# Performance work log

Hardware: AMD Instinct MI355X
Metric: run time of the kernel (lower is better)

## Reference

```python
import jax, jax.numpy as jnp
import numpy as np

Z, Y, X = 32, 480, 480          # sparse voxel grid (LiDAR-scale)
N = 200_000                     # active voxels
C_IN, C_OUT = 64, 64
EPS = 1e-5


def _subm_conv(f, nbr, w):
    """Submanifold sparse conv as gather-matmul-accumulate.
    f: [N, Cin]; nbr: [N, K] neighbor row ids, pad index == N for missing;
    w: [K, Cin, Cout]."""
    f_pad = jnp.concatenate([f, jnp.zeros((1, f.shape[1]), f.dtype)], axis=0)
    g = f_pad[nbr]                       # [N, K, Cin] gathered neighbor features
    return jnp.einsum('nkc,kco->no', g, w)


def _bn(x, gamma, beta):
    # BatchNorm1d in training mode: batch stats over the N dimension
    m = x.mean(axis=0)
    v = x.var(axis=0)
    return (x - m) * jax.lax.rsqrt(v + EPS) * gamma + beta


def setup_inputs() -> dict:
    rng = np.random.default_rng(0)
    ids = rng.choice(Z * Y * X, size=N, replace=False)
    lookup = np.full(Z * Y * X, -1, dtype=np.int64)
    lookup[ids] = np.arange(N)
    z = ids // (Y * X)
    y = (ids // X) % Y
    x = ids % X

    def nbr_table(offsets):
        cols = []
        for dz, dy, dx in offsets:
            zz, yy, xx = z + dz, y + dy, x + dx
            ok = (zz >= 0) & (zz < Z) & (yy >= 0) & (yy < Y) & (xx >= 0) & (xx < X)
            lin = np.clip((zz * Y + yy) * X + xx, 0, Z * Y * X - 1)
            idx = np.where(ok, lookup[lin], -1)
            cols.append(np.where(idx >= 0, idx, N))   # pad index N -> zero row
        return jnp.asarray(np.stack(cols, axis=1).astype(np.int32))

    off13 = [(0, dy, dx) for dy in (-1, 0, 1) for dx in (-1, 0, 1)]  # kernel (1,3,3)
    off31 = [(dz, 0, dx) for dz in (-1, 0, 1) for dx in (-1, 0, 1)]  # kernel (3,1,3)

    key = jax.random.key(0)
    ks = jax.random.split(key, 5)
    s = 0.05
    ones = jnp.ones((C_OUT,), jnp.float32)
    zeros = jnp.zeros((C_OUT,), jnp.float32)
    return {
        'features': jax.random.normal(ks[0], (N, C_IN), jnp.float32),
        'w1':   jax.random.normal(ks[1], (9, C_IN, C_OUT), jnp.float32) * s,
        'w1_2': jax.random.normal(ks[2], (9, C_OUT, C_OUT), jnp.float32) * s,
        'w2':   jax.random.normal(ks[3], (9, C_IN, C_OUT), jnp.float32) * s,
        'w3':   jax.random.normal(ks[4], (9, C_OUT, C_OUT), jnp.float32) * s,
        'g0': ones, 'b0': zeros, 'g0_2': ones, 'b0_2': zeros,
        'g1': ones, 'b1': zeros, 'g2': ones, 'b2': zeros,
        'nbr13': nbr_table(off13),
        'nbr31': nbr_table(off31),
    }


def reference(features, w1, w1_2, w2, w3, g0, b0, g0_2, b0_2, g1, b1, g2, b2,
              nbr13, nbr31):
    # shortcut branch: conv1x3 -> LeakyReLU -> BN -> conv3x1 -> LeakyReLU -> BN
    sc = _subm_conv(features, nbr13, w1)
    sc = _bn(jax.nn.leaky_relu(sc), g0, b0)
    sc = _subm_conv(sc, nbr31, w1_2)
    sc = _bn(jax.nn.leaky_relu(sc), g0_2, b0_2)
    # main branch: conv3x1 -> LeakyReLU -> BN -> conv1x3 -> LeakyReLU -> BN
    r = _subm_conv(features, nbr31, w2)
    r = _bn(jax.nn.leaky_relu(r), g1, b1)
    r = _subm_conv(r, nbr13, w3)
    r = _bn(jax.nn.leaky_relu(r), g2, b2)
    return r + sc
```

## Files before the change

### kernel.cpp

```cpp
#include <hip/hip_runtime.h>

#define NVOX 200000
#define TM 128
#define NBLK 1563
#define NREP 32
#define STG 4224

typedef unsigned short u16;
typedef unsigned int u32;
typedef __bf16 bf16x8 __attribute__((ext_vector_type(8)));
typedef float f32x16 __attribute__((ext_vector_type(16)));

__device__ __forceinline__ float bf2f(u16 h) { return __uint_as_float(((u32)h) << 16); }
__device__ __forceinline__ u16 f2bf(float x) {
  u32 u = __float_as_uint(x);
  u32 r = u + 0x7fffu + ((u >> 16) & 1u);
  return (u16)(r >> 16);
}
__device__ __forceinline__ uint4 cvt8(uint4 a, uint4 b) {
  const float* fa = (const float*)&a;
  const float* fb = (const float*)&b;
  uint4 r;
  u16* q = (u16*)&r;
#pragma unroll
  for (int j = 0; j < 4; ++j) { q[j] = f2bf(fa[j]); q[4 + j] = f2bf(fb[j]); }
  return r;
}

template <int PHASE>
__global__ __launch_bounds__(256, 6)
void conv_fused(const void* __restrict__ inA, const void* __restrict__ inB,
                const int* __restrict__ nbrA, const int* __restrict__ nbrB,
                const u16* __restrict__ wfA, const u16* __restrict__ wfB,
                void* yA, void* yB, float* __restrict__ stA, float* __restrict__ stB) {
  __shared__ __align__(16) float fb4[64 * 68];
  __shared__ float sred[4][128];

  const int tid = threadIdx.x;
  const int bid = blockIdx.x;
  const bool hB = (bid >= NBLK);
  const int blk = hB ? bid - NBLK : bid;
  const void* f = hB ? inB : inA;
  const int* nbr = hB ? nbrB : nbrA;
  const u16* wf = hB ? wfB : wfA;
  float* st = hB ? stB : stA;

  const int wv = tid >> 6;
  const int lane = tid & 63;
  const int lrow = lane & 31;
  const int lq = lane >> 5;
  const int base = blk * TM;
  const int gr = base + wv * 32 + lrow;

  int ids[9];
#pragma unroll
  for (int j = 0; j < 9; ++j) ids[j] = (gr < NVOX) ? nbr[gr * 9 + j] : NVOX;

  f32x16 acc0 = {0.f, 0.f, 0.f, 0.f, 0.f, 0.f, 0.f, 0.f,
                 0.f, 0.f, 0.f, 0.f, 0.f, 0.f, 0.f, 0.f};
  f32x16 acc1 = acc0;
  constexpr bool FOLDED = (PHASE == 1);
  constexpr bool INF32 = (PHASE == 0);
  constexpr int KSTRIDE = FOLDED ? 5120 : 4096;

#pragma unroll
  for (int k = 0; k < 9; ++k) {
    if (k != 4) {
      if (__ballot(ids[k] < NVOX) == 0ull) continue;
    }
    const int id = ids[k];
    const bool ok = id < NVOX;
    uint4 af[4];
    if constexpr (INF32) {
      const float* p = (const float*)f + (size_t)id * 64 + lq * 8;
#pragma unroll
      for (int ksi = 0; ksi < 4; ++ksi) {
        uint4 v0 = make_uint4(0u, 0u, 0u, 0u), v1 = v0;
        if (ok) { v0 = *(const uint4*)(p + ksi * 16); v1 = *(const uint4*)(p + ksi * 16 + 4); }
        af[ksi] = cvt8(v0, v1);
      }
    } else {
      const u16* p = (const u16*)f + (size_t)id * 64 + lq * 8;
#pragma unroll
      for (int ksi = 0; ksi < 4; ++ksi) {
        uint4 v = make_uint4(0u, 0u, 0u, 0u);
        if (ok) v = *(const uint4*)(p + ksi * 16);
        af[ksi] = v;
      }
    }
    const u16* wb = wf + k * KSTRIDE;
#pragma unroll
    for (int ksi = 0; ksi < 4; ++ksi) {
      bf16x8 a = __builtin_bit_cast(bf16x8, af[ksi]);
      bf16x8 b0 = __builtin_bit_cast(bf16x8, *(const uint4*)(wb + (ksi * 2) * 512 + lane * 8));
      bf16x8 b1 = __builtin_bit_cast(bf16x8, *(const uint4*)(wb + (ksi * 2 + 1) * 512 + lane * 8));
      acc0 = __builtin_amdgcn_mfma_f32_32x32x16_bf16(a, b0, acc0, 0, 0, 0);
      acc1 = __builtin_amdgcn_mfma_f32_32x32x16_bf16(a, b1, acc1, 0, 0, 0);
    }
    if constexpr (FOLDED) {
      uint4 a4 = make_uint4(0u, 0u, 0u, 0u);
      if (lq == 0 && ok) ((u16*)&a4)[0] = 0x3F80u;
      bf16x8 a = __builtin_bit_cast(bf16x8, a4);
      bf16x8 b0 = __builtin_bit_cast(bf16x8, *(const uint4*)(wb + 8 * 512 + lane * 8));
      bf16x8 b1 = __builtin_bit_cast(bf16x8, *(const uint4*)(wb + 9 * 512 + lane * 8));
      acc0 = __builtin_amdgcn_mfma_f32_32x32x16_bf16(a, b0, acc0, 0, 0, 0);
      acc1 = __builtin_amdgcn_mfma_f32_32x32x16_bf16(a, b1, acc1, 0, 0, 0);
    }
  }

  const int cc0 = lrow, cc1 = 32 + lrow;
  float s0 = 0.f, q0 = 0.f, s1 = 0.f, q1 = 0.f;
  float vout[2][16];
#pragma unroll
  for (int r = 0; r < 16; ++r) {
    float v = acc0[r]; v = v > 0.f ? v : 0.01f * v;
    s0 += v; q0 += v * v; vout[0][r] = v;
    float w = acc1[r]; w = w > 0.f ? w : 0.01f * w;
    s1 += w; q1 += w * w; vout[1][r] = w;
  }
  s0 += __shfl_xor(s0, 32); q0 += __shfl_xor(q0, 32);
  s1 += __shfl_xor(s1, 32); q1 += __shfl_xor(q1, 32);
  if (lq == 0) {
    sred[wv][lrow] = s0; sred[wv][32 + lrow] = s1;
    sred[wv][64 + lrow] = q0; sred[wv][96 + lrow] = q1;
  }

  const bool f32out = (PHASE == 1) && !hB;
  const int trow = tid >> 3, cp = tid & 7;
  u16* bb = (u16*)fb4;
#pragma unroll
  for (int h = 0; h < 2; ++h) {
    __syncthreads();
    if ((wv >> 1) == h) {
      const int lr = 32 * (wv & 1);
#pragma unroll
      for (int r = 0; r < 16; ++r) {
        int rowD = lr + (r & 3) + 8 * (r >> 2) + 4 * lq;
        if (f32out) {
          fb4[rowD * 68 + cc0] = vout[0][r];
          fb4[rowD * 68 + cc1] = vout[1][r];
        } else {
          bb[rowD * 72 + cc0] = f2bf(vout[0][r]);
          bb[rowD * 72 + cc1] = f2bf(vout[1][r]);
        }
      }
    }
    __syncthreads();
    if (f32out) {
      float* y = (float*)yA;
#pragma unroll
      for (int it = 0; it < 2; ++it) {
        int r = it * 32 + trow, row = base + 64 * h + r;
        if (row < NVOX) {
          *(float4*)(y + (size_t)row * 64 + cp * 8) = *(const float4*)(fb4 + r * 68 + cp * 8);
          *(float4*)(y + (size_t)row * 64 + cp * 8 + 4) = *(const float4*)(fb4 + r * 68 + cp * 8 + 4);
        }
      }
    } else {
      u16* y = (u16*)(hB ? yB : yA);
#pragma unroll
      for (int it = 0; it < 2; ++it) {
        int r = it * 32 + trow, row = base + 64 * h + r;
        if (row < NVOX)
          *(uint4*)(y + (size_t)row * 64 + cp * 8) = *(const uint4*)(bb + r * 72 + cp * 8);
      }
    }
  }
  if (tid < 128) {
    int which = tid >> 6, c = tid & 63;
    float v = sred[0][which * 64 + c] + sred[1][which * 64 + c] +
              sred[2][which * 64 + c] + sred[3][which * 64 + c];
    atomicAdd(&st[(bid & (NREP - 1)) * 128 + which * 64 + c], v);
  }
}

template <bool IN_F32, bool FOLDED, int MODE>
__global__ __launch_bounds__(256, 4)
void conv_k(const void* __restrict__ fv, const int* __restrict__ nbr,
            const u16* __restrict__ wf, void* yv, float* __restrict__ st,
            float* io, const float* __restrict__ affD,
            const float* __restrict__ affB) {
  __shared__ __align__(16) float fb[128 * 68];
  __shared__ float sred[4][128];

  const int tid = threadIdx.x;
  const int wv = tid >> 6;
  const int lane = tid & 63;
  const int lrow = lane & 31;
  const int lq = lane >> 5;
  const int base = blockIdx.x * TM;
  const int gr = base + wv * 32 + lrow;

  int ids[9];
#pragma unroll
  for (int j = 0; j < 9; ++j) ids[j] = (gr < NVOX) ? nbr[gr * 9 + j] : NVOX;

  f32x16 acc0 = {0.f, 0.f, 0.f, 0.f, 0.f, 0.f, 0.f, 0.f,
                 0.f, 0.f, 0.f, 0.f, 0.f, 0.f, 0.f, 0.f};
  f32x16 acc1 = acc0;
  constexpr int KSTRIDE = FOLDED ? 5120 : 4096;

#pragma unroll
  for (int k = 0; k < 9; ++k) {
    if (k != 4) {
      if (__ballot(ids[k] < NVOX) == 0ull) continue;
    }
    const int id = ids[k];
    const bool ok = id < NVOX;
    uint4 af[4];
    if constexpr (IN_F32) {
      const float* p = (const float*)fv + (size_t)id * 64 + lq * 8;
#pragma unroll
      for (int ksi = 0; ksi < 4; ++ksi) {
        uint4 v0 = make_uint4(0u, 0u, 0u, 0u), v1 = v0;
        if (ok) { v0 = *(const uint4*)(p + ksi * 16); v1 = *(const uint4*)(p + ksi * 16 + 4); }
        af[ksi] = cvt8(v0, v1);
      }
    } else {
      const u16* p = (const u16*)fv + (size_t)id * 64 + lq * 8;
#pragma unroll
      for (int ksi = 0; ksi < 4; ++ksi) {
        uint4 v = make_uint4(0u, 0u, 0u, 0u);
        if (ok) v = *(const uint4*)(p + ksi * 16);
        af[ksi] = v;
      }
    }
    const u16* wb = wf + k * KSTRIDE;
#pragma unroll
    for (int ksi = 0; ksi < 4; ++ksi) {
      bf16x8 a = __builtin_bit_cast(bf16x8, af[ksi]);
      bf16x8 b0 = __builtin_bit_cast(bf16x8, *(const uint4*)(wb + (ksi * 2) * 512 + lane * 8));
      bf16x8 b1 = __builtin_bit_cast(bf16x8, *(const uint4*)(wb + (ksi * 2 + 1) * 512 + lane * 8));
      acc0 = __builtin_amdgcn_mfma_f32_32x32x16_bf16(a, b0, acc0, 0, 0, 0);
      acc1 = __builtin_amdgcn_mfma_f32_32x32x16_bf16(a, b1, acc1, 0, 0, 0);
    }
    if constexpr (FOLDED) {
      uint4 a4 = make_uint4(0u, 0u, 0u, 0u);
      if (lq == 0 && ok) ((u16*)&a4)[0] = 0x3F80u;
      bf16x8 a = __builtin_bit_cast(bf16x8, a4);
      bf16x8 b0 = __builtin_bit_cast(bf16x8, *(const uint4*)(wb + 8 * 512 + lane * 8));
      bf16x8 b1 = __builtin_bit_cast(bf16x8, *(const uint4*)(wb + 9 * 512 + lane * 8));
      acc0 = __builtin_amdgcn_mfma_f32_32x32x16_bf16(a, b0, acc0, 0, 0, 0);
      acc1 = __builtin_amdgcn_mfma_f32_32x32x16_bf16(a, b1, acc1, 0, 0, 0);
    }
  }

  const int cc0 = lrow, cc1 = 32 + lrow;
  float aD0 = 0.f, aD1 = 0.f, hD0 = 0.f, hD1 = 0.f;
  if constexpr (MODE == 2) {
    aD0 = affD[cc0]; hD0 = affD[64 + cc0];
    aD1 = affD[cc1]; hD1 = affD[64 + cc1];
  }
  float s0 = 0.f, q0 = 0.f, s1 = 0.f, q1 = 0.f;
  float vout[2][16];
#pragma unroll
  for (int r = 0; r < 16; ++r) {
    float v = acc0[r]; v = v > 0.f ? v : 0.01f * v;
    s0 += v; q0 += v * v; vout[0][r] = v;
    float w = acc1[r]; w = w > 0.f ? w : 0.01f * w;
    s1 += w; q1 += w * w; vout[1][r] = w;
  }
  if constexpr (MODE != 2) {
    s0 += __shfl_xor(s0, 32); q0 += __shfl_xor(q0, 32);
    s1 += __shfl_xor(s1, 32); q1 += __shfl_xor(q1, 32);
    if (lq == 0) {
      sred[wv][lrow] = s0; sred[wv][32 + lrow] = s1;
      sred[wv][64 + lrow] = q0; sred[wv][96 + lrow] = q1;
    }
  }
  if constexpr (MODE == 0) {
    u16* bb = (u16*)fb;
#pragma unroll
    for (int r = 0; r < 16; ++r) {
      int rowD = 32 * wv + (r & 3) + 8 * (r >> 2) + 4 * lq;
      bb[rowD * 72 + cc0] = f2bf(vout[0][r]);
      bb[rowD * 72 + cc1] = f2bf(vout[1][r]);
    }
  } else if constexpr (MODE == 2 || MODE == 3) {
#pragma unroll
    for (int r = 0; r < 16; ++r) {
      int rowD = 32 * wv + (r & 3) + 8 * (r >> 2) + 4 * lq;
      float v0 = vout[0][r], v1 = vout[1][r];
      if constexpr (MODE == 2) { v0 = fmaf(v0, aD0, hD0); v1 = fmaf(v1, aD1, hD1); }
      fb[rowD * 68 + cc0] = v0;
      fb[rowD * 68 + cc1] = v1;
    }
  }
  __syncthreads();

  const int trow = tid >> 3, cp = tid & 7;
  if constexpr (MODE == 0) {
    u16* y = (u16*)yv;
    const u16* bb = (const u16*)fb;
#pragma unroll
    for (int it = 0; it < 4; ++it) {
      int r = it * 32 + trow, row = base + r;
      if (row < NVOX)
        *(uint4*)(y + (size_t)row * 64 + cp * 8) = *(const uint4*)(bb + r * 72 + cp * 8);
    }
  }
  if constexpr (MODE == 3) {
    float* y = (float*)yv;
#pragma unroll
    for (int it = 0; it < 4; ++it) {
      int r = it * 32 + trow, row = base + r;
      if (row < NVOX) {
        *(float4*)(y + (size_t)row * 64 + cp * 8) = *(const float4*)(fb + r * 68 + cp * 8);
        *(float4*)(y + (size_t)row * 64 + cp * 8 + 4) = *(const float4*)(fb + r * 68 + cp * 8 + 4);
      }
    }
  }
  if constexpr (MODE == 2) {
    float* y = (float*)yv;
#pragma unroll
    for (int it = 0; it < 4; ++it) {
      int r = it * 32 + trow, row = base + r;
      if (row < NVOX) {
        float t[8], p[8], o[8];
        *(float4*)&t[0] = *(const float4*)(fb + r * 68 + cp * 8);
        *(float4*)&t[4] = *(const float4*)(fb + r * 68 + cp * 8 + 4);
        *(float4*)&p[0] = *(const float4*)(io + (size_t)row * 64 + cp * 8);
        *(float4*)&p[4] = *(const float4*)(io + (size_t)row * 64 + cp * 8 + 4);
#pragma unroll
        for (int j = 0; j < 8; ++j) {
          int c = cp * 8 + j;
          o[j] = t[j] + fmaf(p[j], affB[c], affB[64 + c]);
        }
        *(float4*)(y + (size_t)row * 64 + cp * 8) = *(const float4*)&o[0];
        *(float4*)(y + (size_t)row * 64 + cp * 8 + 4) = *(const float4*)&o[4];
      }
    }
  }
  if constexpr (MODE != 2) {
    if (tid < 128) {
      int which = tid >> 6, c = tid & 63;
      float v = sred[0][which * 64 + c] + sred[1][which * 64 + c] +
                sred[2][which * 64 + c] + sred[3][which * 64 + c];
      atomicAdd(&st[(blockIdx.x & (NREP - 1)) * 128 + which * 64 + c], v);
    }
  }
}

__global__ void prep_all(const float* __restrict__ feat, const float* __restrict__ w1,
                         const float* __restrict__ w2, u16* __restrict__ wf,
                         u16* __restrict__ F, float* __restrict__ st,
                         int cvt_blocks) {
  const int bid = blockIdx.x, tid = threadIdx.x;
  if (bid < cvt_blocks) {
    int i8 = (bid * 256 + tid) * 8;
    if (i8 < NVOX * 64) {
      uint4 a = *(const uint4*)(feat + i8);
      uint4 b = *(const uint4*)(feat + i8 + 4);
      *(uint4*)(F + i8) = cvt8(a, b);
    }
    return;
  }
  int rb = bid - cvt_blocks;
  if (rb < 288) {
    int e = rb * 256 + tid;
    int slot = e / 36864, r = e % 36864;
    int k = r >> 12, rr = r & 4095;
    int frag = rr >> 9, lane = (rr >> 3) & 63, j = rr & 7;
    int ks = frag >> 1, ct = frag & 1;
    int cin = ks * 16 + (lane >> 5) * 8 + j;
    int cout = ct * 32 + (lane & 31);
    const float* src = slot ? w2 : w1;
    wf[e] = f2bf(src[k * 4096 + cin * 64 + cout]);
    return;
  }
  for (int i = tid; i < 4 * STG; i += 256) st[i] = 0.f;
}

__device__ __forceinline__ void bn_from_replicas(const float* stp, const float* g,
                                                 const float* b, int c,
                                                 float* sc, float* sh) {
  float s = 0.f, q = 0.f;
#pragma unroll
  for (int r = 0; r < NREP; ++r) {
    s += stp[r * 128 + c];
    q += stp[r * 128 + 64 + c];
  }
  const float invn = 1.0f / (float)NVOX;
  float mean = s * invn;
  float var = q * invn - mean * mean;
  float sca = g[c] * rsqrtf(var + 1e-5f);
  *sc = sca;
  *sh = b[c] - mean * sca;
}

__global__ void wscale2(const float* __restrict__ wA, float* __restrict__ stpA,
                        const float* __restrict__ gA, const float* __restrict__ bA,
                        u16* __restrict__ dA,
                        const float* __restrict__ wB, float* __restrict__ stpB,
                        const float* __restrict__ gB, const float* __restrict__ bB,
                        u16* __restrict__ dB) {
  __shared__ float sc[64], sh[64];
  const int tid = threadIdx.x;
  const bool hB = (blockIdx.x >= 180);
  const float* wraw = hB ? wB : wA;
  float* stp = hB ? stpB : stpA;
  const float* g = hB ? gB : gA;
  const float* b = hB ? bB : bA;
  u16* dst = hB ? dB : dA;
  const int blk = hB ? blockIdx.x - 180 : blockIdx.x;
  if (tid < 64) {
    float a, h;
    bn_from_replicas(stp, g, b, tid, &a, &h);
    sc[tid] = a; sh[tid] = h;
    if (blk == 0) { stp[NREP * 128 + tid] = a; stp[NREP * 128 + 64 + tid] = h; }
  }
  __syncthreads();
  int e = blk * 256 + tid;
  int k = e / 5120, r = e % 5120;
  int frag = r >> 9, lane = (r >> 3) & 63, j = r & 7;
  int ks = frag >> 1, ct = frag & 1;
  int cout = ct * 32 + (lane & 31);
  u16 val = 0;
  if (ks < 4) {
    int cin = ks * 16 + (lane >> 5) * 8 + j;
    val = f2bf(sc[cin] * wraw[k * 4096 + cin * 64 + cout]);
  } else if (((lane >> 5) == 0) && j == 0) {
    float acc = 0.f;
    for (int c = 0; c < 64; ++c) acc += sh[c] * wraw[k * 4096 + c * 64 + cout];
    val = f2bf(acc);
  }
  dst[e] = val;
}

__global__ void finalize2(float* __restrict__ stA, const float* __restrict__ gA,
                          const float* __restrict__ bA, float* __restrict__ stB,
                          const float* __restrict__ gB, const float* __restrict__ bB) {
  int t = threadIdx.x;
  float* stp = (t < 64) ? stA : stB;
  const float* g = (t < 64) ? gA : gB;
  const float* b = (t < 64) ? bA : bB;
  int c = t & 63;
  if (t < 128) {
    float a, h;
    bn_from_replicas(stp, g, b, c, &a, &h);
    stp[NREP * 128 + c] = a;
    stp[NREP * 128 + 64 + c] = h;
  }
}

__global__ void final_add(const u16* __restrict__ y3, float* io,
                          const float* __restrict__ affB, const float* __restrict__ affD) {
  int i8 = (blockIdx.x * 256 + threadIdx.x) * 8;
  if (i8 < NVOX * 64) {
    float a[8];
    *(float4*)&a[0] = *(const float4*)(io + i8);
    *(float4*)&a[4] = *(const float4*)(io + i8 + 4);
    uint4 vd = *(const uint4*)(y3 + i8);
    const u16* pd = (const u16*)&vd;
    int cb = i8 & 63;
    float o[8];
#pragma unroll
    for (int j = 0; j < 8; ++j) {
      int c = cb + j;
      o[j] = fmaf(a[j], affB[c], affB[64 + c]) + fmaf(bf2f(pd[j]), affD[c], affD[64 + c]);
    }
    *(float4*)(io + i8) = *(const float4*)&o[0];
    *(float4*)(io + i8 + 4) = *(const float4*)&o[4];
  }
}

__global__ void final_add2(const u16* __restrict__ y3, float* io,
                           float* __restrict__ stB, const float* __restrict__ gB,
                           const float* __restrict__ bB,
                           float* __restrict__ stD, const float* __restrict__ gD,
                           const float* __restrict__ bD) {
  __shared__ float aff[4][64];
  const int t = threadIdx.x;
  if (t < 128) {
    float a, h;
    if (t < 64) { bn_from_replicas(stB, gB, bB, t, &a, &h); aff[0][t] = a; aff[1][t] = h; }
    else { int c = t - 64; bn_from_replicas(stD, gD, bD, c, &a, &h); aff[2][c] = a; aff[3][c] = h; }
  }
  __syncthreads();
  int i8 = (blockIdx.x * 256 + t) * 8;
  if (i8 < NVOX * 64) {
    float a[8];
    *(float4*)&a[0] = *(const float4*)(io + i8);
    *(float4*)&a[4] = *(const float4*)(io + i8 + 4);
    uint4 vd = *(const uint4*)(y3 + i8);
    const u16* pd = (const u16*)&vd;
    int cb = i8 & 63;
    float o[8];
#pragma unroll
    for (int j = 0; j < 8; ++j) {
      int c = cb + j;
      o[j] = fmaf(a[j], aff[0][c], aff[1][c]) + fmaf(bf2f(pd[j]), aff[2][c], aff[3][c]);
    }
    *(float4*)(io + i8) = *(const float4*)&o[0];
    *(float4*)(io + i8 + 4) = *(const float4*)&o[4];
  }
}

extern "C" void kernel_launch(void* const* d_in, const int* in_sizes, int n_in,
                              void* d_out, int out_size, void* d_ws, size_t ws_size,
                              hipStream_t stream) {
  const float* feat = (const float*)d_in[0];
  const float* w1 = (const float*)d_in[1];
  const float* w1_2 = (const float*)d_in[2];
  const float* w2 = (const float*)d_in[3];
  const float* w3 = (const float*)d_in[4];
  const float* g0 = (const float*)d_in[5];
  const float* b0 = (const float*)d_in[6];
  const float* g0_2 = (const float*)d_in[7];
  const float* b0_2 = (const float*)d_in[8];
  const float* g1 = (const float*)d_in[9];
  const float* b1 = (const float*)d_in[10];
  const float* g2 = (const float*)d_in[11];
  const float* b2 = (const float*)d_in[12];
  const int* nbr13 = (const int*)d_in[13];
  const int* nbr31 = (const int*)d_in[14];
  float* out = (float*)d_out;

  char* ws = (char*)d_ws;
  float* st = (float*)ws;
  u16* wf = (u16*)(ws + 67584);
  u16* s0 = wf;
  u16* s1 = wf + 36864;
  u16* s2 = wf + 73728;
  u16* s3 = wf + 119808;
  u16* F = (u16*)(ws + 399488);
  u16* A1 = F + (size_t)NVOX * 64;
  u16* A2 = A1 + (size_t)NVOX * 64;
  const size_t base_sz = 399488;
  const size_t need_fused = base_sz + 3ull * NVOX * 64 * 2;
  const size_t need_serial = base_sz + 2ull * NVOX * 64 * 2;

  float* st0 = st, *st1 = st + STG, *st2 = st + 2 * STG, *st3 = st + 3 * STG;

  if (ws_size >= need_fused) {
    prep_all<<<289, 256, 0, stream>>>(feat, w1, w2, wf, F, st, 0);
    conv_fused<0><<<2 * NBLK, 256, 0, stream>>>(feat, feat, nbr13, nbr31, s0, s1,
                                                A1, A2, st0, st2);
    wscale2<<<360, 256, 0, stream>>>(w1_2, st0, g0, b0, s2, w3, st2, g1, b1, s3);
    conv_fused<1><<<2 * NBLK, 256, 0, stream>>>(A1, A2, nbr31, nbr13, s2, s3,
                                                out, F, st1, st3);
    final_add2<<<6250, 256, 0, stream>>>(F, out, st1, g0_2, b0_2, st3, g2, b2);
  } else if (ws_size >= need_serial) {
    prep_all<<<6539, 256, 0, stream>>>(feat, w1, w2, wf, F, st, 6250);
    conv_k<false, false, 0><<<NBLK, 256, 0, stream>>>(F, nbr13, s0, A1, st0, nullptr, nullptr, nullptr);
    wscale2<<<180, 256, 0, stream>>>(w1_2, st0, g0, b0, s2, w3, st2, g1, b1, s3);
    conv_k<false, true, 3><<<NBLK, 256, 0, stream>>>(A1, nbr31, s2, out, st1, nullptr, nullptr, nullptr);
    conv_k<false, false, 0><<<NBLK, 256, 0, stream>>>(F, nbr31, s1, A1, st2, nullptr, nullptr, nullptr);
    wscale2<<<360, 256, 0, stream>>>(w1_2, st0, g0, b0, s2, w3, st2, g1, b1, s3);
    conv_k<false, true, 0><<<NBLK, 256, 0, stream>>>(A1, nbr13, s3, F, st3, nullptr, nullptr, nullptr);
    finalize2<<<1, 128, 0, stream>>>(st1, g0_2, b0_2, st3, g2, b2);
    final_add<<<6250, 256, 0, stream>>>(F, out, st1 + NREP * 128, st3 + NREP * 128);
  } else {
    u16* Az = F;
    prep_all<<<289, 256, 0, stream>>>(feat, w1, w2, wf, nullptr, st, 0);
    conv_k<true, false, 0><<<NBLK, 256, 0, stream>>>(feat, nbr13, s0, Az, st0, nullptr, nullptr, nullptr);
    wscale2<<<180, 256, 0, stream>>>(w1_2, st0, g0, b0, s2, w3, st2, g1, b1, s3);
    conv_k<false, true, 3><<<NBLK, 256, 0, stream>>>(Az, nbr31, s2, out, st1, nullptr, nullptr, nullptr);
    finalize2<<<1, 128, 0, stream>>>(st1, g0_2, b0_2, st3, g2, b2);
    conv_k<true, false, 0><<<NBLK, 256, 0, stream>>>(feat, nbr31, s1, Az, st2, nullptr, nullptr, nullptr);
    wscale2<<<360, 256, 0, stream>>>(w1_2, st0, g0, b0, s2, w3, st2, g1, b1, s3);
    conv_k<false, true, 1><<<NBLK, 256, 0, stream>>>(Az, nbr13, s3, nullptr, st3, nullptr, nullptr, nullptr);
    finalize2<<<1, 128, 0, stream>>>(st1, g0_2, b0_2, st3, g2, b2);
    conv_k<false, true, 2><<<NBLK, 256, 0, stream>>>(Az, nbr13, s3, out, nullptr, out,
                                                     st3 + NREP * 128, st1 + NREP * 128);
  }
}
```

Baseline: 273.8 us.

## Fuse all stages into one cooperative persistent kernel with grid syncs

Replaces the five separate launches of the fused path with a single cooperative kernel. The kernel runs prep, the first conv pair, weight scaling, the second conv pair and the final BN-add as grid-stride loops separated by grid.sync. The first conv now reads the pre-converted bf16 features instead of converting fp32 on the fly, and prep converts the full feature tensor. This removes launch gaps and tail effects between stages, at the cost of grid-wide barrier overhead, a persistent grid size limited by occupancy, and an extra full conversion pass over the features.

```diff
diff --git a/kernel.cpp b/kernel.cpp
--- a/kernel.cpp
+++ b/kernel.cpp
@@ -1,4 +1,7 @@
 #include <hip/hip_runtime.h>
+#include <hip/hip_cooperative_groups.h>
+
+namespace cg = cooperative_groups;
 
 #define NVOX 200000
 #define TM 128
@@ -27,20 +30,72 @@
   return r;
 }
 
+__device__ __forceinline__ void bn_from_replicas(const float* stp, const float* g,
+                                                 const float* b, int c,
+                                                 float* sc, float* sh) {
+  float s = 0.f, q = 0.f;
+#pragma unroll
+  for (int r = 0; r < NREP; ++r) {
+    s += stp[r * 128 + c];
+    q += stp[r * 128 + 64 + c];
+  }
+  const float invn = 1.0f / (float)NVOX;
+  float mean = s * invn;
+  float var = q * invn - mean * mean;
+  float sca = g[c] * rsqrtf(var + 1e-5f);
+  *sc = sca;
+  *sh = b[c] - mean * sca;
+}
+
+struct MegaParams {
+  const float* feat;
+  const float* w1; const float* w1_2; const float* w2; const float* w3;
+  const float* g0; const float* b0; const float* g0_2; const float* b0_2;
+  const float* g1; const float* b1; const float* g2; const float* b2;
+  const int* nbr13; const int* nbr31;
+  float* out;
+  float* stats; float* st0; float* st1; float* st2; float* st3;
+  u16* wf; u16* s0; u16* s1; u16* s2; u16* s3;
+  u16* F; u16* A1; u16* A2;
+};
+
+__device__ void prep_body(int bid, const MegaParams& p) {
+  const int tid = threadIdx.x;
+  if (bid < 6250) {
+    int i8 = (bid * 256 + tid) * 8;
+    if (i8 < NVOX * 64) {
+      uint4 a = *(const uint4*)(p.feat + i8);
+      uint4 b = *(const uint4*)(p.feat + i8 + 4);
+      *(uint4*)(p.F + i8) = cvt8(a, b);
+    }
+    return;
+  }
+  int rb = bid - 6250;
+  if (rb < 288) {
+    int e = rb * 256 + tid;
+    int slot = e / 36864, r = e % 36864;
+    int k = r >> 12, rr = r & 4095;
+    int frag = rr >> 9, lane = (rr >> 3) & 63, j = rr & 7;
+    int ks = frag >> 1, ct = frag & 1;
+    int cin = ks * 16 + (lane >> 5) * 8 + j;
+    int cout = ct * 32 + (lane & 31);
+    const float* src = slot ? p.w2 : p.w1;
+    p.wf[e] = f2bf(src[k * 4096 + cin * 64 + cout]);
+    return;
+  }
+  for (int i = tid; i < 4 * STG; i += 256) p.stats[i] = 0.f;
+}
+
 template <int PHASE>
-__global__ __launch_bounds__(256, 6)
-void conv_fused(const void* __restrict__ inA, const void* __restrict__ inB,
-                const int* __restrict__ nbrA, const int* __restrict__ nbrB,
-                const u16* __restrict__ wfA, const u16* __restrict__ wfB,
-                void* yA, void* yB, float* __restrict__ stA, float* __restrict__ stB) {
-  __shared__ __align__(16) float fb4[64 * 68];
-  __shared__ float sred[4][128];
-
+__device__ void conv_body(int bid, const u16* inA, const u16* inB,
+                          const int* nbrA, const int* nbrB,
+                          const u16* wfA, const u16* wfB,
+                          void* yA, void* yB, float* stA, float* stB,
+                          float* fb4, float (*sred)[128]) {
   const int tid = threadIdx.x;
-  const int bid = blockIdx.x;
   const bool hB = (bid >= NBLK);
   const int blk = hB ? bid - NBLK : bid;
-  const void* f = hB ? inB : inA;
+  const u16* f = hB ? inB : inA;
   const int* nbr = hB ? nbrB : nbrA;
   const u16* wf = hB ? wfB : wfA;
   float* st = hB ? stB : stA;
@@ -60,7 +115,6 @@
                  0.f, 0.f, 0.f, 0.f, 0.f, 0.f, 0.f, 0.f};
   f32x16 acc1 = acc0;
   constexpr bool FOLDED = (PHASE == 1);
-  constexpr bool INF32 = (PHASE == 0);
   constexpr int KSTRIDE = FOLDED ? 5120 : 4096;
 
 #pragma unroll
@@ -71,22 +125,12 @@
     const int id = ids[k];
     const bool ok = id < NVOX;
     uint4 af[4];
-    if constexpr (INF32) {
-      const float* p = (const float*)f + (size_t)id * 64 + lq * 8;
-#pragma unroll
-      for (int ksi = 0; ksi < 4; ++ksi) {
-        uint4 v0 = make_uint4(0u, 0u, 0u, 0u), v1 = v0;
-        if (ok) { v0 = *(const uint4*)(p + ksi * 16); v1 = *(const uint4*)(p + ksi * 16 + 4); }
-        af[ksi] = cvt8(v0, v1);
-      }
-    } else {
-      const u16* p = (const u16*)f + (size_t)id * 64 + lq * 8;
-#pragma unroll
-      for (int ksi = 0; ksi < 4; ++ksi) {
-        uint4 v = make_uint4(0u, 0u, 0u, 0u);
-        if (ok) v = *(const uint4*)(p + ksi * 16);
-        af[ksi] = v;
-      }
+    const u16* pp = f + (size_t)id * 64 + lq * 8;
+#pragma unroll
+    for (int ksi = 0; ksi < 4; ++ksi) {
+      uint4 v = make_uint4(0u, 0u, 0u, 0u);
+      if (ok) v = *(const uint4*)(pp + ksi * 16);
+      af[ksi] = v;
     }
     const u16* wb = wf + k * KSTRIDE;
 #pragma unroll
@@ -172,6 +216,99 @@
               sred[2][which * 64 + c] + sred[3][which * 64 + c];
     atomicAdd(&st[(bid & (NREP - 1)) * 128 + which * 64 + c], v);
   }
+  __syncthreads();
+}
+
+__device__ void wscale_body(int blkid, const MegaParams& p, float* smem) {
+  float* sc = smem;
+  float* sh = smem + 64;
+  const int tid = threadIdx.x;
+  const bool hB = (blkid >= 180);
+  const float* wraw = hB ? p.w3 : p.w1_2;
+  float* stp = hB ? p.st2 : p.st0;
+  const float* g = hB ? p.g1 : p.g0;
+  const float* b = hB ? p.b1 : p.b0;
+  u16* dst = hB ? p.s3 : p.s2;
+  const int blk = hB ? blkid - 180 : blkid;
+  if (tid < 64) {
+    float a, h;
+    bn_from_replicas(stp, g, b, tid, &a, &h);
+    sc[tid] = a; sh[tid] = h;
+  }
+  __syncthreads();
+  int e = blk * 256 + tid;
+  int k = e / 5120, r = e % 5120;
+  int frag = r >> 9, lane = (r >> 3) & 63, j = r & 7;
+  int ks = frag >> 1, ct = frag & 1;
+  int cout = ct * 32 + (lane & 31);
+  u16 val = 0;
+  if (ks < 4) {
+    int cin = ks * 16 + (lane >> 5) * 8 + j;
+    val = f2bf(sc[cin] * wraw[k * 4096 + cin * 64 + cout]);
+  } else if (((lane >> 5) == 0) && j == 0) {
+    float acc = 0.f;
+    for (int c = 0; c < 64; ++c) acc += sh[c] * wraw[k * 4096 + c * 64 + cout];
+    val = f2bf(acc);
+  }
+  dst[e] = val;
+  __syncthreads();
+}
+
+__device__ void final_body(const MegaParams& p, float* smem, int nb) {
+  float* aff = smem;
+  const int t = threadIdx.x;
+  if (t < 128) {
+    float a, h;
+    if (t < 64) {
+      bn_from_replicas(p.st1, p.g0_2, p.b0_2, t, &a, &h);
+      aff[t] = a; aff[64 + t] = h;
+    } else {
+      int c = t - 64;
+      bn_from_replicas(p.st3, p.g2, p.b2, c, &a, &h);
+      aff[128 + c] = a; aff[192 + c] = h;
+    }
+  }
+  __syncthreads();
+  for (int b = blockIdx.x; b < 6250; b += nb) {
+    int i8 = (b * 256 + t) * 8;
+    if (i8 < NVOX * 64) {
+      float a[8];
+      *(float4*)&a[0] = *(const float4*)(p.out + i8);
+      *(float4*)&a[4] = *(const float4*)(p.out + i8 + 4);
+      uint4 vd = *(const uint4*)(p.F + i8);
+      const u16* pd = (const u16*)&vd;
+      int cb = i8 & 63;
+      float o[8];
+#pragma unroll
+      for (int j = 0; j < 8; ++j) {
+        int c = cb + j;
+        o[j] = fmaf(a[j], aff[c], aff[64 + c]) + fmaf(bf2f(pd[j]), aff[128 + c], aff[192 + c]);
+      }
+      *(float4*)(p.out + i8) = *(const float4*)&o[0];
+      *(float4*)(p.out + i8 + 4) = *(const float4*)&o[4];
+    }
+  }
+}
+
+__global__ __launch_bounds__(256, 6) void mega(MegaParams p) {
+  __shared__ __align__(16) float fb4[64 * 68];
+  __shared__ float sred[4][128];
+  cg::grid_group grid = cg::this_grid();
+  const int nb = gridDim.x;
+
+  for (int b = blockIdx.x; b < 6539; b += nb) prep_body(b, p);
+  grid.sync();
+  for (int b = blockIdx.x; b < 2 * NBLK; b += nb)
+    conv_body<0>(b, p.F, p.F, p.nbr13, p.nbr31, p.s0, p.s1,
+                 p.A1, p.A2, p.st0, p.st2, fb4, sred);
+  grid.sync();
+  for (int b = blockIdx.x; b < 360; b += nb) wscale_body(b, p, fb4);
+  grid.sync();
+  for (int b = blockIdx.x; b < 2 * NBLK; b += nb)
+    conv_body<1>(b, p.A1, p.A2, p.nbr31, p.nbr13, p.s2, p.s3,
+                 p.out, p.F, p.st1, p.st3, fb4, sred);
+  grid.sync();
+  final_body(p, fb4, nb);
 }
 
 template <bool IN_F32, bool FOLDED, int MODE>
@@ -316,15 +453,15 @@
     for (int it = 0; it < 4; ++it) {
       int r = it * 32 + trow, row = base + r;
       if (row < NVOX) {
-        float t[8], p[8], o[8];
+        float t[8], pp[8], o[8];
         *(float4*)&t[0] = *(const float4*)(fb + r * 68 + cp * 8);
         *(float4*)&t[4] = *(const float4*)(fb + r * 68 + cp * 8 + 4);
-        *(float4*)&p[0] = *(const float4*)(io + (size_t)row * 64 + cp * 8);
-        *(float4*)&p[4] = *(const float4*)(io + (size_t)row * 64 + cp * 8 + 4);
+        *(float4*)&pp[0] = *(const float4*)(io + (size_t)row * 64 + cp * 8);
+        *(float4*)&pp[4] = *(const float4*)(io + (size_t)row * 64 + cp * 8 + 4);
 #pragma unroll
         for (int j = 0; j < 8; ++j) {
           int c = cp * 8 + j;
-          o[j] = t[j] + fmaf(p[j], affB[c], affB[64 + c]);
+          o[j] = t[j] + fmaf(pp[j], affB[c], affB[64 + c]);
         }
         *(float4*)(y + (size_t)row * 64 + cp * 8) = *(const float4*)&o[0];
         *(float4*)(y + (size_t)row * 64 + cp * 8 + 4) = *(const float4*)&o[4];
@@ -369,23 +506,6 @@
     return;
   }
   for (int i = tid; i < 4 * STG; i += 256) st[i] = 0.f;
-}
-
-__device__ __forceinline__ void bn_from_replicas(const float* stp, const float* g,
-                                                 const float* b, int c,
-                                                 float* sc, float* sh) {
-  float s = 0.f, q = 0.f;
-#pragma unroll
-  for (int r = 0; r < NREP; ++r) {
-    s += stp[r * 128 + c];
-    q += stp[r * 128 + 64 + c];
-  }
-  const float invn = 1.0f / (float)NVOX;
-  float mean = s * invn;
-  float var = q * invn - mean * mean;
-  float sca = g[c] * rsqrtf(var + 1e-5f);
-  *sc = sca;
-  *sh = b[c] - mean * sca;
 }
 
 __global__ void wscale2(const float* __restrict__ wA, float* __restrict__ stpA,
@@ -464,38 +584,6 @@
   }
 }
 
-__global__ void final_add2(const u16* __restrict__ y3, float* io,
-                           float* __restrict__ stB, const float* __restrict__ gB,
-                           const float* __restrict__ bB,
-                           float* __restrict__ stD, const float* __restrict__ gD,
-                           const float* __restrict__ bD) {
-  __shared__ float aff[4][64];
-  const int t = threadIdx.x;
-  if (t < 128) {
-    float a, h;
-    if (t < 64) { bn_from_replicas(stB, gB, bB, t, &a, &h); aff[0][t] = a; aff[1][t] = h; }
-    else { int c = t - 64; bn_from_replicas(stD, gD, bD, c, &a, &h); aff[2][c] = a; aff[3][c] = h; }
-  }
-  __syncthreads();
-  int i8 = (blockIdx.x * 256 + t) * 8;
-  if (i8 < NVOX * 64) {
-    float a[8];
-    *(float4*)&a[0] = *(const float4*)(io + i8);
-    *(float4*)&a[4] = *(const float4*)(io + i8 + 4);
-    uint4 vd = *(const uint4*)(y3 + i8);
-    const u16* pd = (const u16*)&vd;
-    int cb = i8 & 63;
-    float o[8];
-#pragma unroll
-    for (int j = 0; j < 8; ++j) {
-      int c = cb + j;
-      o[j] = fmaf(a[j], aff[0][c], aff[1][c]) + fmaf(bf2f(pd[j]), aff[2][c], aff[3][c]);
-    }
-    *(float4*)(io + i8) = *(const float4*)&o[0];
-    *(float4*)(io + i8 + 4) = *(const float4*)&o[4];
-  }
-}
-
 extern "C" void kernel_launch(void* const* d_in, const int* in_sizes, int n_in,
                               void* d_out, int out_size, void* d_ws, size_t ws_size,
                               hipStream_t stream) {
@@ -533,13 +621,31 @@
   float* st0 = st, *st1 = st + STG, *st2 = st + 2 * STG, *st3 = st + 3 * STG;
 
   if (ws_size >= need_fused) {
-    prep_all<<<289, 256, 0, stream>>>(feat, w1, w2, wf, F, st, 0);
-    conv_fused<0><<<2 * NBLK, 256, 0, stream>>>(feat, feat, nbr13, nbr31, s0, s1,
-                                                A1, A2, st0, st2);
-    wscale2<<<360, 256, 0, stream>>>(w1_2, st0, g0, b0, s2, w3, st2, g1, b1, s3);
-    conv_fused<1><<<2 * NBLK, 256, 0, stream>>>(A1, A2, nbr31, nbr13, s2, s3,
-                                                out, F, st1, st3);
-    final_add2<<<6250, 256, 0, stream>>>(F, out, st1, g0_2, b0_2, st3, g2, b2);
+    static int coopGrid = 0;
+    if (coopGrid == 0) {
+      int maxb = 0;
+      hipOccupancyMaxActiveBlocksPerMultiprocessor(&maxb, mega, 256, 0);
+      if (maxb <= 0) maxb = 4;
+      int dev = 0;
+      hipGetDevice(&dev);
+      hipDeviceProp_t prop;
+      int ncu = 256;
+      if (hipGetDeviceProperties(&prop, dev) == hipSuccess && prop.multiProcessorCount > 0)
+        ncu = prop.multiProcessorCount;
+      coopGrid = maxb * ncu;
+      if (coopGrid > 6539) coopGrid = 6539;
+    }
+    MegaParams p;
+    p.feat = feat; p.w1 = w1; p.w1_2 = w1_2; p.w2 = w2; p.w3 = w3;
+    p.g0 = g0; p.b0 = b0; p.g0_2 = g0_2; p.b0_2 = b0_2;
+    p.g1 = g1; p.b1 = b1; p.g2 = g2; p.b2 = b2;
+    p.nbr13 = nbr13; p.nbr31 = nbr31; p.out = out;
+    p.stats = st; p.st0 = st0; p.st1 = st1; p.st2 = st2; p.st3 = st3;
+    p.wf = wf; p.s0 = s0; p.s1 = s1; p.s2 = s2; p.s3 = s3;
+    p.F = F; p.A1 = A1; p.A2 = A2;
+    void* kargs[] = {(void*)&p};
+    hipLaunchCooperativeKernel((const void*)mega, dim3(coopGrid), dim3(256),
+                               kargs, 0, stream);
   } else if (ws_size >= need_serial) {
     prep_all<<<6539, 256, 0, stream>>>(feat, w1, w2, wf, F, st, 6250);
     conv_k<false, false, 0><<<NBLK, 256, 0, stream>>>(F, nbr13, s0, A1, st0, nullptr, nullptr, nullptr);
```

Measured after the change: 744.3 us. 2.72x slower.
